# Optimization experiments

Hardware: AMD Instinct MI355X
Metric: run time of the kernel (lower is better)

## Reference

```python
import jax, jax.numpy as jnp
import numpy as np

B, P, D = 8, 4096, 3  # B point clouds, P points each, 3-D coords (code slices [:, :3])


def setup_inputs() -> dict:
    key = jax.random.key(0)
    k1, k2 = jax.random.split(key)
    y1 = jax.random.normal(k1, (B * P, D), dtype=jnp.float32)
    y2 = jax.random.normal(k2, (B * P, D), dtype=jnp.float32)
    # Sorted, equal-sized contiguous batch ids (as produced by PyG DataLoader batching).
    b1 = jnp.repeat(jnp.arange(B, dtype=jnp.int32), P)
    b2 = jnp.repeat(jnp.arange(B, dtype=jnp.int32), P)
    return {"y1": y1, "y2": y2, "b1": b1, "b2": b2}


def _chamfer(y1, y2):
    # Batch ids are contiguous with equal counts -> reshape to [B, P, D];
    # knn with batch args restricts neighbors to the same cloud.
    a = y1.reshape(B, P, D)
    c = y2.reshape(B, P, D)
    aa = jnp.sum(a * a, axis=-1)                      # [B, P]
    cc = jnp.sum(c * c, axis=-1)                      # [B, P]
    # Squared pairwise distances per cloud: [B, P, P]
    sq = aa[:, :, None] + cc[:, None, :] - 2.0 * jnp.einsum('bpd,bqd->bpq', a, c)
    # k=1 NN of each y1 point in y2 (argmin over y2 axis)
    idx1 = jnp.argmin(sq, axis=2)                     # [B, P]
    nn1 = jnp.take_along_axis(c, idx1[..., None], axis=1)  # [B, P, D]
    d1 = jnp.mean(jnp.linalg.norm(a - nn1, axis=-1))
    # k=1 NN of each y2 point in y1 (argmin over y1 axis)
    idx2 = jnp.argmin(sq, axis=1)                     # [B, P]
    nn2 = jnp.take_along_axis(a, idx2[..., None], axis=1)  # [B, P, D]
    d2 = jnp.mean(jnp.linalg.norm(c - nn2, axis=-1))
    return d1 + d2


def reference(y1, y2, b1, b2):
    # b1/b2 encode the contiguous equal-size batch structure assumed above.
    return _chamfer(y1, y2)
```

## Files before the change

kernel.cpp:

```cpp
#include <hip/hip_runtime.h>
#include <float.h>
#include <math.h>

#define BB 8
#define PP 4096

typedef __attribute__((ext_vector_type(8))) short bf16x8;
typedef __attribute__((ext_vector_type(16))) float f32x16;

__device__ __forceinline__ unsigned int f2bf(float f) {
    unsigned int u = __float_as_uint(f);
    return (u + 0x7FFFu + ((u >> 16) & 1u)) >> 16;
}
__device__ __forceinline__ float bf2f(unsigned int h) {
    return __uint_as_float(h << 16);
}
__device__ __forceinline__ float min3f(float a, float b, float c) {
    return fminf(fminf(a, b), c);
}

__global__ __launch_bounds__(1024) void chamfer_mfma(
    const float* __restrict__ y1, const float* __restrict__ y2,
    float* __restrict__ partial)
{
    __shared__ uint4 fbuf[64 * 64];

    const int bid   = blockIdx.x;
    const int qg    = bid & 15;
    const int cloud = (bid >> 4) & 7;
    const int dir   = bid >> 7;

    const float* src = (dir == 0) ? y1 : y2;
    const float* tgt = (dir == 0) ? y2 : y1;
    const float* __restrict__ tgt_base = tgt + (size_t)cloud * PP * 3;
    const float* __restrict__ src_base = src + ((size_t)cloud * PP + (size_t)qg * 256) * 3;

    const int tid  = threadIdx.x;
    const int lane = tid & 63;
    const int w    = tid >> 6;
    const int ig   = w & 7;
    const int jh   = w >> 3;

    bf16x8 bfrag;
    {
        const int ql = ig * 32 + (lane & 31);
        const float ax = src_base[ql * 3 + 0];
        const float ay = src_base[ql * 3 + 1];
        const float az = src_base[ql * 3 + 2];
        const unsigned int hx = f2bf(-ax), hy = f2bf(-ay), hz = f2bf(-az);
        const unsigned int lx = f2bf(-ax - bf2f(hx));
        const unsigned int ly = f2bf(-ay - bf2f(hy));
        const unsigned int lz = f2bf(-az - bf2f(hz));
        uint4 bb;
        if (lane < 32) {
            bb.x = hx | (hy << 16);
            bb.y = hz | (lx << 16);
            bb.z = ly | (lz << 16);
            bb.w = hx | (hy << 16);
        } else {
            bb.x = hz | (0x3F80u << 16);
            bb.y = 0x3F80u;
            bb.z = 0u;
            bb.w = 0u;
        }
        bfrag = *reinterpret_cast<bf16x8*>(&bb);
    }

    float m0 = FLT_MAX, m1 = FLT_MAX, m2 = FLT_MAX, m3 = FLT_MAX;

    f32x16 zc;
    #pragma unroll
    for (int r = 0; r < 16; ++r) zc[r] = 0.0f;

#define FOLD(acc)                              \
    do {                                       \
        m0 = min3f(m0, (acc)[0], (acc)[4]);    \
        m1 = min3f(m1, (acc)[1], (acc)[5]);    \
        m2 = min3f(m2, (acc)[2], (acc)[6]);    \
        m3 = min3f(m3, (acc)[3], (acc)[7]);    \
        m0 = min3f(m0, (acc)[8], (acc)[12]);   \
        m1 = min3f(m1, (acc)[9], (acc)[13]);   \
        m2 = min3f(m2, (acc)[10], (acc)[14]);  \
        m3 = min3f(m3, (acc)[11], (acc)[15]);  \
    } while (0)

    for (int half = 0; half < 2; ++half) {
        #pragma unroll
        for (int rep = 0; rep < 2; ++rep) {
            const int nl = rep * 1024 + tid;
            const int n  = half * 2048 + nl;
            const float cx = tgt_base[n * 3 + 0];
            const float cy = tgt_base[n * 3 + 1];
            const float cz = tgt_base[n * 3 + 2];
            const unsigned int chx = f2bf(cx), chy = f2bf(cy), chz = f2bf(cz);
            const unsigned int clx = f2bf(cx - bf2f(chx));
            const unsigned int cly = f2bf(cy - bf2f(chy));
            const unsigned int clz = f2bf(cz - bf2f(chz));
            const float hh = 0.5f * (cx * cx + cy * cy + cz * cz);
            const unsigned int hhi = f2bf(hh);
            const unsigned int hlo = f2bf(hh - bf2f(hhi));
            const int tile = nl >> 5, r = nl & 31;
            uint4 lof, hif;
            lof.x = chx | (chy << 16);
            lof.y = chz | (chx << 16);
            lof.z = chy | (chz << 16);
            lof.w = clx | (cly << 16);
            hif.x = clz | (hhi << 16);
            hif.y = hlo;
            hif.z = 0u;
            hif.w = 0u;
            fbuf[tile * 64 + r]      = lof;
            fbuf[tile * 64 + 32 + r] = hif;
        }
        __syncthreads();

        const uint4* __restrict__ fb = &fbuf[(size_t)(jh * 32) * 64 + lane];
        bf16x8 afA = *reinterpret_cast<const bf16x8*>(fb);
        f32x16 accA = __builtin_amdgcn_mfma_f32_32x32x16_bf16(afA, bfrag, zc, 0, 0, 0);
        bf16x8 afB;
        f32x16 accB;
        for (int jt = 1; jt < 31; jt += 2) {
            afB  = *reinterpret_cast<const bf16x8*>(fb + (size_t)jt * 64);
            accB = __builtin_amdgcn_mfma_f32_32x32x16_bf16(afB, bfrag, zc, 0, 0, 0);
            FOLD(accA);
            afA  = *reinterpret_cast<const bf16x8*>(fb + (size_t)(jt + 1) * 64);
            accA = __builtin_amdgcn_mfma_f32_32x32x16_bf16(afA, bfrag, zc, 0, 0, 0);
            FOLD(accB);
        }
        afB  = *reinterpret_cast<const bf16x8*>(fb + (size_t)31 * 64);
        accB = __builtin_amdgcn_mfma_f32_32x32x16_bf16(afB, bfrag, zc, 0, 0, 0);
        FOLD(accA);
        FOLD(accB);
        __syncthreads();
    }
#undef FOLD

    float* pmin = reinterpret_cast<float*>(fbuf);
    float* ssum = pmin + 512;
    {
        float mm = fminf(fminf(m0, m1), fminf(m2, m3));
        mm = fminf(mm, __shfl_xor(mm, 32));
        if (lane < 32)
            pmin[jh * 256 + ig * 32 + (lane & 31)] = mm;
    }
    __syncthreads();
    if (tid < 256) {
        float v = fminf(pmin[tid], pmin[256 + tid]);
        const float ax = src_base[tid * 3 + 0];
        const float ay = src_base[tid * 3 + 1];
        const float az = src_base[tid * 3 + 2];
        const float aa = ax * ax + ay * ay + az * az;
        float d = sqrtf(fmaxf(0.0f, fmaf(2.0f, v, aa)));
        #pragma unroll
        for (int off = 32; off > 0; off >>= 1)
            d += __shfl_down(d, off);
        if ((tid & 63) == 0)
            ssum[tid >> 6] = d;
    }
    __syncthreads();
    if (tid == 0)
        partial[bid] = ssum[0] + ssum[1] + ssum[2] + ssum[3];
}

__global__ __launch_bounds__(256) void chamfer_final(
    const float* __restrict__ partial, float* __restrict__ out)
{
    __shared__ float ssum[4];
    const int tid = threadIdx.x;
    float v = partial[tid];
    #pragma unroll
    for (int off = 32; off > 0; off >>= 1)
        v += __shfl_down(v, off);
    if ((tid & 63) == 0)
        ssum[tid >> 6] = v;
    __syncthreads();
    if (tid == 0)
        out[0] = (ssum[0] + ssum[1] + ssum[2] + ssum[3]) * (1.0f / (float)(BB * PP));
}

extern "C" void kernel_launch(void* const* d_in, const int* in_sizes, int n_in,
                              void* d_out, int out_size, void* d_ws, size_t ws_size,
                              hipStream_t stream) {
    const float* y1 = (const float*)d_in[0];
    const float* y2 = (const float*)d_in[1];
    float* partial = (float*)d_ws;
    float* out     = (float*)d_out;

    chamfer_mfma<<<256, 1024, 0, stream>>>(y1, y2, partial);
    chamfer_final<<<1, 256, 0, stream>>>(partial, out);
}
```

Before: 17.43 us.

## Precompute bf16 target fragments once and stream them into LDS via global_load_lds

Adds a pre-pass kernel that converts each target cloud into split-bf16 MFMA fragments once, writing them to workspace. Before, each of the 16 query-group blocks per cloud redid that conversion. The main kernel now copies the prebuilt fragments directly into LDS with global_load_lds, and the MFMA loop is simplified to issue two independent MFMAs per iteration. The cost is an extra kernel launch and roughly 2 MB of workspace traffic in exchange for less redundant ALU work and direct global-to-LDS copies.

```diff
diff --git a/kernel.cpp b/kernel.cpp
--- a/kernel.cpp
+++ b/kernel.cpp
@@ -19,9 +19,46 @@
     return fminf(fminf(a, b), c);
 }
 
+__global__ __launch_bounds__(256) void build_frags(
+    const float* __restrict__ y1, const float* __restrict__ y2,
+    uint4* __restrict__ frags)
+{
+    const int gid   = blockIdx.x * 256 + threadIdx.x;
+    const int cs    = gid >> 12;
+    const int n     = gid & 4095;
+    const int dir   = cs >> 3;
+    const int cloud = cs & 7;
+    const float* tgt = (dir == 0) ? y2 : y1;
+    const float* g = tgt + ((size_t)cloud * PP + n) * 3;
+
+    const float cx = g[0], cy = g[1], cz = g[2];
+    const unsigned int chx = f2bf(cx), chy = f2bf(cy), chz = f2bf(cz);
+    const unsigned int clx = f2bf(cx - bf2f(chx));
+    const unsigned int cly = f2bf(cy - bf2f(chy));
+    const unsigned int clz = f2bf(cz - bf2f(chz));
+    const float hh = 0.5f * (cx * cx + cy * cy + cz * cz);
+    const unsigned int hhi = f2bf(hh);
+    const unsigned int hlo = f2bf(hh - bf2f(hhi));
+
+    uint4 lof, hif;
+    lof.x = chx | (chy << 16);
+    lof.y = chz | (chx << 16);
+    lof.z = chy | (chz << 16);
+    lof.w = clx | (cly << 16);
+    hif.x = clz | (hhi << 16);
+    hif.y = hlo;
+    hif.z = 0u;
+    hif.w = 0u;
+
+    const int half = n >> 11, nl = n & 2047, tile = nl >> 5, r = nl & 31;
+    uint4* dst = frags + ((size_t)cs * 8192 + (size_t)half * 4096 + (size_t)tile * 64);
+    dst[r]      = lof;
+    dst[32 + r] = hif;
+}
+
 __global__ __launch_bounds__(1024) void chamfer_mfma(
     const float* __restrict__ y1, const float* __restrict__ y2,
-    float* __restrict__ partial)
+    const uint4* __restrict__ frags, float* __restrict__ partial)
 {
     __shared__ uint4 fbuf[64 * 64];
 
@@ -29,10 +66,9 @@
     const int qg    = bid & 15;
     const int cloud = (bid >> 4) & 7;
     const int dir   = bid >> 7;
+    const int cs    = bid >> 4;
 
     const float* src = (dir == 0) ? y1 : y2;
-    const float* tgt = (dir == 0) ? y2 : y1;
-    const float* __restrict__ tgt_base = tgt + (size_t)cloud * PP * 3;
     const float* __restrict__ src_base = src + ((size_t)cloud * PP + (size_t)qg * 256) * 3;
 
     const int tid  = threadIdx.x;
@@ -85,52 +121,27 @@
     } while (0)
 
     for (int half = 0; half < 2; ++half) {
+        const uint4* __restrict__ gsrc = frags + ((size_t)cs * 8192 + (size_t)half * 4096);
         #pragma unroll
-        for (int rep = 0; rep < 2; ++rep) {
-            const int nl = rep * 1024 + tid;
-            const int n  = half * 2048 + nl;
-            const float cx = tgt_base[n * 3 + 0];
-            const float cy = tgt_base[n * 3 + 1];
-            const float cz = tgt_base[n * 3 + 2];
-            const unsigned int chx = f2bf(cx), chy = f2bf(cy), chz = f2bf(cz);
-            const unsigned int clx = f2bf(cx - bf2f(chx));
-            const unsigned int cly = f2bf(cy - bf2f(chy));
-            const unsigned int clz = f2bf(cz - bf2f(chz));
-            const float hh = 0.5f * (cx * cx + cy * cy + cz * cz);
-            const unsigned int hhi = f2bf(hh);
-            const unsigned int hlo = f2bf(hh - bf2f(hhi));
-            const int tile = nl >> 5, r = nl & 31;
-            uint4 lof, hif;
-            lof.x = chx | (chy << 16);
-            lof.y = chz | (chx << 16);
-            lof.z = chy | (chz << 16);
-            lof.w = clx | (cly << 16);
-            hif.x = clz | (hhi << 16);
-            hif.y = hlo;
-            hif.z = 0u;
-            hif.w = 0u;
-            fbuf[tile * 64 + r]      = lof;
-            fbuf[tile * 64 + 32 + r] = hif;
+        for (int r = 0; r < 4; ++r) {
+            const int chunk = r * 16 + w;
+            const uint4* gp = gsrc + chunk * 64 + lane;
+            uint4* lp = &fbuf[chunk * 64];
+            __builtin_amdgcn_global_load_lds(
+                (const __attribute__((address_space(1))) uint4*)gp,
+                (__attribute__((address_space(3))) uint4*)lp, 16, 0, 0);
         }
         __syncthreads();
 
         const uint4* __restrict__ fb = &fbuf[(size_t)(jh * 32) * 64 + lane];
-        bf16x8 afA = *reinterpret_cast<const bf16x8*>(fb);
-        f32x16 accA = __builtin_amdgcn_mfma_f32_32x32x16_bf16(afA, bfrag, zc, 0, 0, 0);
-        bf16x8 afB;
-        f32x16 accB;
-        for (int jt = 1; jt < 31; jt += 2) {
-            afB  = *reinterpret_cast<const bf16x8*>(fb + (size_t)jt * 64);
-            accB = __builtin_amdgcn_mfma_f32_32x32x16_bf16(afB, bfrag, zc, 0, 0, 0);
-            FOLD(accA);
-            afA  = *reinterpret_cast<const bf16x8*>(fb + (size_t)(jt + 1) * 64);
-            accA = __builtin_amdgcn_mfma_f32_32x32x16_bf16(afA, bfrag, zc, 0, 0, 0);
-            FOLD(accB);
+        for (int jt = 0; jt < 32; jt += 2) {
+            const bf16x8 a0 = *reinterpret_cast<const bf16x8*>(fb + (size_t)jt * 64);
+            const bf16x8 a1 = *reinterpret_cast<const bf16x8*>(fb + (size_t)(jt + 1) * 64);
+            f32x16 acc0 = __builtin_amdgcn_mfma_f32_32x32x16_bf16(a0, bfrag, zc, 0, 0, 0);
+            f32x16 acc1 = __builtin_amdgcn_mfma_f32_32x32x16_bf16(a1, bfrag, zc, 0, 0, 0);
+            FOLD(acc0);
+            FOLD(acc1);
         }
-        afB  = *reinterpret_cast<const bf16x8*>(fb + (size_t)31 * 64);
-        accB = __builtin_amdgcn_mfma_f32_32x32x16_bf16(afB, bfrag, zc, 0, 0, 0);
-        FOLD(accA);
-        FOLD(accB);
         __syncthreads();
     }
 #undef FOLD
@@ -183,9 +194,11 @@
                               hipStream_t stream) {
     const float* y1 = (const float*)d_in[0];
     const float* y2 = (const float*)d_in[1];
-    float* partial = (float*)d_ws;
+    uint4* frags   = (uint4*)d_ws;
+    float* partial = (float*)((char*)d_ws + (1 << 21));
     float* out     = (float*)d_out;
 
-    chamfer_mfma<<<256, 1024, 0, stream>>>(y1, y2, partial);
+    build_frags<<<256, 256, 0, stream>>>(y1, y2, frags);
+    chamfer_mfma<<<256, 1024, 0, stream>>>(y1, y2, frags, partial);
     chamfer_final<<<1, 256, 0, stream>>>(partial, out);
 }
```

Result: slower. 23.52 us (+35.0%).
